# Kernel tuning notes

Measured on AMD Instinct MI355X. Metric: run time of the kernel, lower is better.

The kernel has to match this reference:

```python
import jax, jax.numpy as jnp
import numpy as np

B = 16
Dv, Hv, Wv = 128, 128, 128   # patchsize voxel grid (C=1)
NPTS = 1920                  # 16*120 points
EPS_IN = 1e-5                # InstanceNorm eps


def _inorm(x):
    # InstanceNorm1d, affine=False: normalize over last (length) dim per (b, c)
    m = jnp.mean(x, axis=-1, keepdims=True)
    v = jnp.var(x, axis=-1, keepdims=True)
    return (x - m) * jax.lax.rsqrt(v + EPS_IN)


def _mlp(q, w1, b1, w2, b2, w3, b3, w4, b4, w5, b5):
    b = q.shape[0]
    x = q.reshape(b, 256, 8)                                    # (b, 2048//8, 8)
    x = jnp.einsum('bil,oi->bol', x, w1) + b1[None, :, None]    # Conv1d(256,240,1) -> (b,240,8)
    x = jax.nn.relu(_inorm(x.reshape(b, 64, 30)))               # view (b,64,30), IN(64)
    # Conv1d(64,128,1,groups=64): each in-ch -> 2 out-chs; then view (b,32,120)
    x = (x[:, :, None, :] * w2[None, :, :, None] + b2.reshape(1, 64, 2, 1)).reshape(b, 32, 120)
    x = jax.nn.relu(_inorm(x))
    # Conv1d(32,64,1,groups=32); view (b,16,480)
    x = (x[:, :, None, :] * w3[None, :, :, None] + b3.reshape(1, 32, 2, 1)).reshape(b, 16, 480)
    x = jax.nn.relu(_inorm(x))
    # Conv1d(16,64,1,groups=16); view (b,16,1920)
    x = (x[:, :, None, :] * w4[None, :, :, None] + b4.reshape(1, 16, 4, 1)).reshape(b, 16, 1920)
    x = jax.nn.relu(_inorm(x))
    return jnp.einsum('bil,oi->bol', x, w5) + b5[None, :, None]  # Conv1d(16,3,1) -> (b,3,1920)


def _splat(vals, grid):
    # True adjoint of 3D grid_sample (align_corners=False, zeros padding):
    # trilinear scatter-add of point values into the voxel grid.
    # vals: (b, N); grid: (b, N, 3) with (x, y, z) ~ (W, H, D) normalized coords.
    b, n = vals.shape
    px = ((grid[..., 0] + 1.0) * Wv - 1.0) * 0.5
    py = ((grid[..., 1] + 1.0) * Hv - 1.0) * 0.5
    pz = ((grid[..., 2] + 1.0) * Dv - 1.0) * 0.5
    x0f = jnp.floor(px); y0f = jnp.floor(py); z0f = jnp.floor(pz)
    fx = px - x0f; fy = py - y0f; fz = pz - z0f
    x0 = x0f.astype(jnp.int32); y0 = y0f.astype(jnp.int32); z0 = z0f.astype(jnp.int32)
    bidx = jnp.arange(b, dtype=jnp.int32)[:, None]
    out = jnp.zeros(b * Dv * Hv * Wv, dtype=vals.dtype)
    for dz in (0, 1):
        wz = fz if dz else (1.0 - fz)
        for dy in (0, 1):
            wy = fy if dy else (1.0 - fy)
            for dx in (0, 1):
                wx = fx if dx else (1.0 - fx)
                xi = x0 + dx; yi = y0 + dy; zi = z0 + dz
                w = wx * wy * wz * vals
                valid = (xi >= 0) & (xi < Wv) & (yi >= 0) & (yi < Hv) & (zi >= 0) & (zi < Dv)
                w = jnp.where(valid, w, 0.0)
                xi = jnp.clip(xi, 0, Wv - 1)
                yi = jnp.clip(yi, 0, Hv - 1)
                zi = jnp.clip(zi, 0, Dv - 1)
                flat = ((bidx * Dv + zi) * Hv + yi) * Wv + xi
                out = out.at[flat.ravel()].add(w.ravel())
    return out.reshape(b, 1, Dv, Hv, Wv)


def _avgpool3(x):
    # AvgPool3d(3, stride=1, padding=1, count_include_pad=True) as separable 1D averages
    for ax in (2, 3, 4):
        pad = [(1, 1) if i == ax else (0, 0) for i in range(5)]
        xp = jnp.pad(x, pad)
        n = x.shape[ax]
        x = (jax.lax.slice_in_dim(xp, 0, n, axis=ax)
             + jax.lax.slice_in_dim(xp, 1, n + 1, axis=ax)
             + jax.lax.slice_in_dim(xp, 2, n + 2, axis=ax)) / 3.0
    return x


def _smooth(x):
    return _avgpool3(_avgpool3(_avgpool3(x)))


def _forward(q, q_val, w1, b1, w2, b2, w3, b3, w4, b4, w5, b5):
    b = q.shape[0]
    q3 = _mlp(q, w1, b1, w2, b2, w3, b3, w4, b4, w5, b5)   # (b, 3, 1920)
    coords = jnp.tanh(q3)                                    # q0_coord
    grid = jnp.transpose(coords, (0, 2, 1))                  # (b, 1920, 3)
    vals = jnp.broadcast_to(jax.nn.sigmoid(q_val).reshape(1, NPTS), (b, NPTS))
    out = _splat(vals, grid)
    out0 = _splat(jnp.ones((b, NPTS), q.dtype), grid)
    return _smooth(out) / (_smooth(out0) + 0.001)


def setup_inputs() -> dict:
    key = jax.random.key(0)
    ks = jax.random.split(key, 12)
    sc = 0.1
    return {
        'q': jax.random.normal(ks[0], (B, 2048), jnp.float32),
        'q_val': jax.random.normal(ks[1], (1, 1, 16, 120), jnp.float32),
        'w1': jax.random.normal(ks[2], (240, 256), jnp.float32) * sc,
        'b1': jax.random.normal(ks[3], (240,), jnp.float32) * sc,
        'w2': jax.random.normal(ks[4], (64, 2), jnp.float32) * sc,
        'b2': jax.random.normal(ks[5], (128,), jnp.float32) * sc,
        'w3': jax.random.normal(ks[6], (32, 2), jnp.float32) * sc,
        'b3': jax.random.normal(ks[7], (64,), jnp.float32) * sc,
        'w4': jax.random.normal(ks[8], (16, 4), jnp.float32) * sc,
        'b4': jax.random.normal(ks[9], (64,), jnp.float32) * sc,
        'w5': jax.random.normal(ks[10], (3, 16), jnp.float32) * sc,
        'b5': jax.random.normal(ks[11], (3,), jnp.float32) * sc,
    }


def reference(q, q_val, w1, b1, w2, b2, w3, b3, w4, b4, w5, b5):
    return _forward(q, q_val, w1, b1, w2, b2, w3, b3, w4, b4, w5, b5)
```

## Files before the change

### kernel.cpp

```cpp
#include <hip/hip_runtime.h>
#include <cstddef>

#define NB 16
#define NVOX 128
#define NPT 1920

static __device__ __forceinline__ float2 f2(float a, float b) {
    float2 r; r.x = a; r.y = b; return r;
}

__device__ __forceinline__ void coef(int g, float& cm1, float& c0, float& cp1)
{
    cm1 = (g == 1 || g == 127) ? 5.f : 6.f;
    c0  = (g == 0 || g == 127) ? 4.f : 7.f;
    cp1 = (g == 0 || g == 126) ? 5.f : 6.f;
}

__global__ __launch_bounds__(256)
void zero_out(float4* __restrict__ out)
{
    int idx = blockIdx.x * 2048 + threadIdx.x;
    #pragma unroll
    for (int i = 0; i < 8; ++i)
        out[idx + i * 256] = make_float4(0.f, 0.f, 0.f, 0.f);
}

__global__ __launch_bounds__(1024)
void tail_k(const float* __restrict__ q, const float* __restrict__ w1,
            const float* __restrict__ b1, const float* __restrict__ qval,
            const float* __restrict__ w2, const float* __restrict__ b2,
            const float* __restrict__ w3, const float* __restrict__ b3,
            const float* __restrict__ w4, const float* __restrict__ b4,
            const float* __restrict__ w5, const float* __restrict__ b5,
            float4* __restrict__ pts, int* __restrict__ bcount,
            int* __restrict__ list)
{
    __shared__ float x1s[1920];
    __shared__ float h3[7680];
    __shared__ float m4s[16], r4s[16];
    __shared__ unsigned char lflags[2048];
    __shared__ int lcount;

    const int b = blockIdx.x;
    const int t = threadIdx.x;
    float* qs = h3;

    for (int u = t; u < 2048; u += 1024) {
        qs[u] = q[b * 2048 + u];
        lflags[u] = 0;
    }
    if (t == 0) lcount = 0;
    __syncthreads();

    for (int u = t; u < 1920; u += 1024) {
        int o = u >> 3, l = u & 7;
        const float4* wr = (const float4*)(w1 + o * 256);
        float acc = 0.f;
        #pragma unroll 8
        for (int i4 = 0; i4 < 64; ++i4) {
            float4 w = wr[i4];
            int base = i4 * 32 + l;
            acc = fmaf(w.x, qs[base],      acc);
            acc = fmaf(w.y, qs[base + 8],  acc);
            acc = fmaf(w.z, qs[base + 16], acc);
            acc = fmaf(w.w, qs[base + 24], acc);
        }
        x1s[u] = b1[o] + acc;
    }
    __syncthreads();

    const int l = t & 63;
    const int c1l = l >> 4;
    const int p16 = l & 15;
    const bool hasb = (p16 < 14);
    {
        const int c3 = t >> 6;
        const int c1 = 4 * c3 + c1l;
        const float* xrow = x1s + c1 * 30;
        float a0 = xrow[p16];
        float a1 = hasb ? xrow[p16 + 16] : 0.f;

        float s = a0 + a1, s2 = a0 * a0 + a1 * a1;
        #pragma unroll
        for (int m = 1; m <= 8; m <<= 1) {
            s  += __shfl_xor(s,  m);
            s2 += __shfl_xor(s2, m);
        }
        float mean = s * (1.f / 30.f);
        float var  = s2 * (1.f / 30.f) - mean * mean;
        float rstd = rsqrtf(var + 1e-5f);
        a0 = fmaxf((a0 - mean) * rstd, 0.f);
        a1 = fmaxf((a1 - mean) * rstd, 0.f);

        const float w20 = w2[c1 * 2 + 0], w21 = w2[c1 * 2 + 1];
        const float b20 = b2[c1 * 2 + 0], b21 = b2[c1 * 2 + 1];
        float y00 = fmaf(a0, w20, b20), y01 = fmaf(a0, w21, b21);
        float y10 = fmaf(a1, w20, b20), y11 = fmaf(a1, w21, b21);

        float u1 = y00 + y01 + (hasb ? (y10 + y11) : 0.f);
        float u2 = y00 * y00 + y01 * y01
                 + (hasb ? (y10 * y10 + y11 * y11) : 0.f);
        #pragma unroll
        for (int m = 1; m <= 16; m <<= 1) {
            u1 += __shfl_xor(u1, m);
            u2 += __shfl_xor(u2, m);
        }
        mean = u1 * (1.f / 120.f);
        var  = u2 * (1.f / 120.f) - mean * mean;
        rstd = rsqrtf(var + 1e-5f);
        y00 = fmaxf((y00 - mean) * rstd, 0.f);
        y01 = fmaxf((y01 - mean) * rstd, 0.f);
        y10 = fmaxf((y10 - mean) * rstd, 0.f);
        y11 = fmaxf((y11 - mean) * rstd, 0.f);

        const int c2 = c1 >> 1;
        const float w30 = w3[c2 * 2 + 0], w31 = w3[c2 * 2 + 1];
        const float b30 = b3[c2 * 2 + 0], b31 = b3[c2 * 2 + 1];
        float z000 = fmaf(y00, w30, b30), z001 = fmaf(y00, w31, b31);
        float z010 = fmaf(y01, w30, b30), z011 = fmaf(y01, w31, b31);
        float z100 = fmaf(y10, w30, b30), z101 = fmaf(y10, w31, b31);
        float z110 = fmaf(y11, w30, b30), z111 = fmaf(y11, w31, b31);

        float v1 = z000 + z001 + z010 + z011
                 + (hasb ? (z100 + z101 + z110 + z111) : 0.f);
        float v2 = z000 * z000 + z001 * z001 + z010 * z010 + z011 * z011
                 + (hasb ? (z100 * z100 + z101 * z101
                          + z110 * z110 + z111 * z111) : 0.f);
        #pragma unroll
        for (int m = 1; m <= 32; m <<= 1) {
            v1 += __shfl_xor(v1, m);
            v2 += __shfl_xor(v2, m);
        }
        mean = v1 * (1.f / 480.f);
        var  = v2 * (1.f / 480.f) - mean * mean;
        rstd = rsqrtf(var + 1e-5f);

        const int qb0 = (c1l >> 1) * 240;
        const int pb0 = (c1l & 1) * 60;
        float* hw = h3 + c3 * 480;
        float s4 = 0.f, q4 = 0.f;
        {
            float v;
            v = fmaxf((z000 - mean) * rstd, 0.f); hw[qb0 +       pb0 +      p16] = v; s4 += v; q4 += v * v;
            v = fmaxf((z001 - mean) * rstd, 0.f); hw[qb0 + 120 + pb0 +      p16] = v; s4 += v; q4 += v * v;
            v = fmaxf((z010 - mean) * rstd, 0.f); hw[qb0 +       pb0 + 30 + p16] = v; s4 += v; q4 += v * v;
            v = fmaxf((z011 - mean) * rstd, 0.f); hw[qb0 + 120 + pb0 + 30 + p16] = v; s4 += v; q4 += v * v;
            if (hasb) {
                v = fmaxf((z100 - mean) * rstd, 0.f); hw[qb0 +       pb0 +      p16 + 16] = v; s4 += v; q4 += v * v;
                v = fmaxf((z101 - mean) * rstd, 0.f); hw[qb0 + 120 + pb0 +      p16 + 16] = v; s4 += v; q4 += v * v;
                v = fmaxf((z110 - mean) * rstd, 0.f); hw[qb0 +       pb0 + 30 + p16 + 16] = v; s4 += v; q4 += v * v;
                v = fmaxf((z111 - mean) * rstd, 0.f); hw[qb0 + 120 + pb0 + 30 + p16 + 16] = v; s4 += v; q4 += v * v;
            }
        }
        #pragma unroll
        for (int m = 1; m <= 32; m <<= 1) {
            s4 += __shfl_xor(s4, m);
            q4 += __shfl_xor(q4, m);
        }
        if (l == 0) {
            float sum4 = 0.f, sq4 = 0.f;
            #pragma unroll
            for (int j = 0; j < 4; ++j) {
                float ww = w4[c3 * 4 + j], bb = b4[c3 * 4 + j];
                sum4 += ww * s4 + 480.f * bb;
                sq4  += ww * ww * q4 + 2.f * ww * bb * s4 + 480.f * bb * bb;
            }
            float m4 = sum4 * (1.f / 1920.f);
            float var4 = sq4 * (1.f / 1920.f) - m4 * m4;
            m4s[c3] = m4; r4s[c3] = rsqrtf(var4 + 1e-5f);
        }
    }
    __syncthreads();

    for (int p = t; p < NPT; p += 1024) {
        int j = p / 480;
        int pp = p - j * 480;
        float a0e = b5[0], a1e = b5[1], a2e = b5[2];
        #pragma unroll
        for (int c = 0; c < 16; ++c) {
            float xv = h3[c * 480 + pp];
            float x4 = fmaf(xv, w4[c * 4 + j], b4[c * 4 + j]);
            float h  = fmaxf((x4 - m4s[c]) * r4s[c], 0.f);
            a0e = fmaf(w5[c],      h, a0e);
            a1e = fmaf(w5[16 + c], h, a1e);
            a2e = fmaf(w5[32 + c], h, a2e);
        }
        float px = tanhf(a0e) * 64.f + 63.5f;
        float py = tanhf(a1e) * 64.f + 63.5f;
        float pz = tanhf(a2e) * 64.f + 63.5f;
        float val = 1.f / (1.f + expf(-qval[p]));

        float4 pv; pv.x = px; pv.y = py; pv.z = pz; pv.w = val;
        pts[b * NPT + p] = pv;

        int x0 = (int)floorf(px), y0 = (int)floorf(py), z0 = (int)floorf(pz);
        int xlo = max(0, x0 - 3), xhi = min(127, x0 + 4);
        int ylo = max(0, y0 - 3), yhi = min(127, y0 + 4);
        int zlo = max(0, z0 - 3), zhi = min(127, z0 + 4);
        if (xlo > xhi || ylo > yhi || zlo > zhi) continue;
        int pxl = xlo >> 4, pxh = xhi >> 4;
        int tyl = ylo >> 3, tyh = yhi >> 3;
        int tzl = zlo >> 3, tzh = zhi >> 3;
        for (int tz = tzl; tz <= tzh; ++tz)
            for (int ty = tyl; ty <= tyh; ++ty)
                for (int px2 = pxl; px2 <= pxh; ++px2)
                    lflags[(tz * 16 + ty) * 8 + px2] = 1;
    }
    __syncthreads();

    for (int u = t; u < 2048; u += 1024) {
        if (lflags[u]) {
            int pos = atomicAdd(&lcount, 1);
            list[b * 2048 + pos] = (b << 11) | u;
        }
    }
    __syncthreads();
    if (t == 0) bcount[b] = lcount;
}

__device__ __forceinline__ void decode_tile(const int* pf, const int* __restrict__ list,
                                            int idx, int& Tx, int& Ty, int& Tz, int& pb_)
{
    int bb = 0;
    #pragma unroll 1
    for (; bb < 15; ++bb) if (idx < pf[bb + 1]) break;
    int code = list[bb * 2048 + (idx - pf[bb])];
    pb_ = code >> 11;
    Tx = (code & 7) * 16;
    Ty = ((code >> 3) & 15) * 8;
    Tz = ((code >> 7) & 15) * 8;
}

__device__ __forceinline__ void zero_buf(float2* raw, int th, int stride)
{
    float4* rz = (float4*)raw;
    for (int u = th; u < 2156; u += stride)
        rz[u] = make_float4(0.f, 0.f, 0.f, 0.f);
}

__device__ __forceinline__ void scatter(float2* raw, const float4* __restrict__ pbp,
                                        int lo, int hi, int th, int stride,
                                        int Tx, int Ty, int Tz)
{
    for (int p = lo + th; p < hi; p += stride) {
        float4 pt = pbp[p];
        float x0f = floorf(pt.x), y0f = floorf(pt.y), z0f = floorf(pt.z);
        int x0 = (int)x0f, y0 = (int)y0f, z0 = (int)z0f;
        int lx0 = x0 - Tx + 3, ly0 = y0 - Ty + 3, lz0 = z0 - Tz + 3;
        if (lx0 + 1 < 0 || lx0 > 21 || ly0 + 1 < 0 || ly0 > 13 ||
            lz0 + 1 < 0 || lz0 > 13) continue;
        float fx = pt.x - x0f, fy = pt.y - y0f, fz = pt.z - z0f;
        float val = pt.w;
        #pragma unroll
        for (int dz = 0; dz < 2; ++dz) {
            int zi = z0 + dz, lz = lz0 + dz;
            if ((unsigned)zi >= 128u || (unsigned)lz >= 14u) continue;
            float wz = dz ? fz : 1.f - fz;
            #pragma unroll
            for (int dy = 0; dy < 2; ++dy) {
                int yi = y0 + dy, ly = ly0 + dy;
                if ((unsigned)yi >= 128u || (unsigned)ly >= 14u) continue;
                float wy = dy ? fy : 1.f - fy;
                #pragma unroll
                for (int dx = 0; dx < 2; ++dx) {
                    int xi = x0 + dx, lx = lx0 + dx;
                    if ((unsigned)xi >= 128u || (unsigned)lx >= 22u) continue;
                    float w = (dx ? fx : 1.f - fx) * wy * wz;
                    float2* cell = &raw[(lz * 14 + ly) * 22 + lx];
                    atomicAdd(&cell->x, w * val);
                    atomicAdd(&cell->y, w);
                }
            }
        }
    }
}

__device__ __forceinline__ void zpass(float2* raw, int Tz, int th)
{
    for (int c = th; c < 308; c += 256) {
        float2 w0 = raw[c],            w1_ = raw[c + 308],
               w2_ = raw[c + 2 * 308], w3_ = raw[c + 3 * 308],
               w4_ = raw[c + 4 * 308], w5_ = raw[c + 5 * 308],
               w6_ = raw[c + 6 * 308];
        #pragma unroll
        for (int z = 0; z < 8; ++z) {
            float cm1, c0, cp1; coef(Tz + z, cm1, c0, cp1);
            float sx = (w0.x + w6_.x) + 3.f * (w1_.x + w5_.x)
                     + cm1 * w2_.x + c0 * w3_.x + cp1 * w4_.x;
            float sy = (w0.y + w6_.y) + 3.f * (w1_.y + w5_.y)
                     + cm1 * w2_.y + c0 * w3_.y + cp1 * w4_.y;
            float2 nxt = raw[c + ((z < 7) ? z + 7 : 7) * 308];
            raw[c + z * 308] = f2(sx * (1.f / 27.f), sy * (1.f / 27.f));
            w0 = w1_; w1_ = w2_; w2_ = w3_; w3_ = w4_; w4_ = w5_; w5_ = w6_; w6_ = nxt;
        }
    }
}

__device__ __forceinline__ void ypass(float2* raw, int Ty, int th)
{
    if (th < 176) {
        int z = th / 22, lx = th - z * 22;
        float2* base = &raw[z * 308 + lx];
        float2 w0 = base[0],       w1_ = base[22],
               w2_ = base[2 * 22], w3_ = base[3 * 22],
               w4_ = base[4 * 22], w5_ = base[5 * 22],
               w6_ = base[6 * 22];
        #pragma unroll
        for (int y = 0; y < 8; ++y) {
            float cm1, c0, cp1; coef(Ty + y, cm1, c0, cp1);
            float sx = (w0.x + w6_.x) + 3.f * (w1_.x + w5_.x)
                     + cm1 * w2_.x + c0 * w3_.x + cp1 * w4_.x;
            float sy = (w0.y + w6_.y) + 3.f * (w1_.y + w5_.y)
                     + cm1 * w2_.y + c0 * w3_.y + cp1 * w4_.y;
            float2 nxt = base[((y < 7) ? y + 7 : 7) * 22];
            base[y * 22] = f2(sx * (1.f / 27.f), sy * (1.f / 27.f));
            w0 = w1_; w1_ = w2_; w2_ = w3_; w3_ = w4_; w4_ = w5_; w5_ = w6_; w6_ = nxt;
        }
    }
}

__device__ __forceinline__ void xpass(float2* raw, int Tx, float* __restrict__ ob, int th)
{
    if (th < 128) {
        int row = th >> 1, hx = th & 1;
        int z = row >> 3, y = row & 7;
        const float2* a = &raw[z * 308 + y * 22 + hx * 8];
        float2 w0 = a[0], w1_ = a[1], w2_ = a[2], w3_ = a[3],
               w4_ = a[4], w5_ = a[5], w6_ = a[6];
        float res[8];
        #pragma unroll
        for (int i = 0; i < 8; ++i) {
            int x = hx * 8 + i;
            float cm1, c0, cp1; coef(Tx + x, cm1, c0, cp1);
            float sx = (w0.x + w6_.x) + 3.f * (w1_.x + w5_.x)
                     + cm1 * w2_.x + c0 * w3_.x + cp1 * w4_.x;
            float sy = (w0.y + w6_.y) + 3.f * (w1_.y + w5_.y)
                     + cm1 * w2_.y + c0 * w3_.y + cp1 * w4_.y;
            res[i] = (sx * (1.f / 27.f)) / (sy * (1.f / 27.f) + 0.001f);
            float2 nxt = a[(i < 7) ? i + 7 : 13];
            w0 = w1_; w1_ = w2_; w2_ = w3_; w3_ = w4_; w4_ = w5_; w5_ = w6_; w6_ = nxt;
        }
        float* orow = &ob[((size_t)z * NVOX + y) * NVOX + hx * 8];
        *(float4*)&orow[0] = make_float4(res[0], res[1], res[2], res[3]);
        *(float4*)&orow[4] = make_float4(res[4], res[5], res[6], res[7]);
    }
}

__global__ __launch_bounds__(512, 4)
void tile_k(const float4* __restrict__ pts, const int* __restrict__ bcount,
            const int* __restrict__ list, float* __restrict__ out)
{
    __shared__ float2 bufA[4312];
    __shared__ float2 bufB[4312];
    __shared__ int pf[17];

    const int t = threadIdx.x;
    if (t < 16) pf[t + 1] = bcount[t];
    if (t == 0) pf[0] = 0;
    __syncthreads();
    if (t == 0) {
        int s = 0;
        #pragma unroll
        for (int i = 1; i <= 16; ++i) { s += pf[i]; pf[i] = s; }
    }
    __syncthreads();

    const int total = pf[16];
    const int grid = gridDim.x;
    const int chunk = (total + grid - 1) / grid;
    int idx = blockIdx.x * chunk;
    const int end = min(idx + chunk, total);
    if (idx >= end) return;

    int cTx, cTy, cTz, cPb;
    decode_tile(pf, list, idx, cTx, cTy, cTz, cPb);
    float2* cur = bufA;
    float2* nxt = bufB;

    zero_buf(cur, t, 512);
    __syncthreads();
    scatter(cur, pts + cPb * NPT, 0, NPT, t, 512, cTx, cTy, cTz);
    __syncthreads();

    const int w8 = t >> 6;
    const bool low = (w8 < 4);
    const int th = t & 255;

    while (true) {
        const bool have_next = (idx + 1) < end;
        int nTx = 0, nTy = 0, nTz = 0, nPb = 0;
        if (have_next)
            decode_tile(pf, list, idx + 1, nTx, nTy, nTz, nPb);

        if (low) zpass(cur, cTz, th);
        else if (have_next) zero_buf(nxt, th, 256);
        __syncthreads();

        if (low) ypass(cur, cTy, th);
        else if (have_next)
            scatter(nxt, pts + nPb * NPT, 0, 960, th, 256, nTx, nTy, nTz);
        __syncthreads();

        if (low) {
            float* ob = out + (((size_t)(cPb * NVOX + cTz) * NVOX + cTy) * NVOX + cTx);
            xpass(cur, cTx, ob, th);
        } else if (have_next)
            scatter(nxt, pts + nPb * NPT, 960, NPT, th, 256, nTx, nTy, nTz);
        __syncthreads();

        if (!have_next) break;
        ++idx;
        float2* tmp = cur; cur = nxt; nxt = tmp;
        cTx = nTx; cTy = nTy; cTz = nTz; cPb = nPb;
    }
}

extern "C" void kernel_launch(void* const* d_in, const int* in_sizes, int n_in,
                              void* d_out, int out_size, void* d_ws, size_t ws_size,
                              hipStream_t stream)
{
    const float* q    = (const float*)d_in[0];
    const float* qval = (const float*)d_in[1];
    const float* w1   = (const float*)d_in[2];
    const float* b1   = (const float*)d_in[3];
    const float* w2   = (const float*)d_in[4];
    const float* b2   = (const float*)d_in[5];
    const float* w3   = (const float*)d_in[6];
    const float* b3   = (const float*)d_in[7];
    const float* w4   = (const float*)d_in[8];
    const float* b4   = (const float*)d_in[9];
    const float* w5   = (const float*)d_in[10];
    const float* b5   = (const float*)d_in[11];
    float* out = (float*)d_out;

    int*    bcount = (int*)d_ws;
    int*    list   = (int*)((char*)d_ws + 64);
    float4* pts    = (float4*)((char*)d_ws + 131136);

    zero_out<<<4096, 256, 0, stream>>>((float4*)out);

    tail_k<<<NB, 1024, 0, stream>>>(q, w1, b1, qval, w2, b2, w3, b3,
                                    w4, b4, w5, b5, pts, bcount, list);

    tile_k<<<512, 512, 0, stream>>>(pts, bcount, list, out);
}
```

Baseline: 242.7 us.

## Bin points per tile with CSR lists and fuse output zeroing into tail kernel

The tail kernel now counts points per output tile, builds prefix offsets and per-tile point index lists (CSR), so the tile kernel scatters only the relevant points instead of scanning all 1920 points per tile. The separate zeroing kernel is folded into extra blocks of the tail kernel, and the double-buffered producer/consumer tile pipeline is replaced by a simpler single-buffer loop with a larger grid. This cuts redundant point loads and bounds checks and one launch, at the cost of shared atomics for binning, extra workspace and the loss of scatter/filter overlap.

```diff
diff --git a/kernel.cpp b/kernel.cpp
--- a/kernel.cpp
+++ b/kernel.cpp
@@ -16,38 +16,42 @@
     cp1 = (g == 0 || g == 126) ? 5.f : 6.f;
 }
 
-__global__ __launch_bounds__(256)
-void zero_out(float4* __restrict__ out)
+__global__ __launch_bounds__(1024)
+void tail_zero_k(const float* __restrict__ q, const float* __restrict__ w1,
+                 const float* __restrict__ b1, const float* __restrict__ qval,
+                 const float* __restrict__ w2, const float* __restrict__ b2,
+                 const float* __restrict__ w3, const float* __restrict__ b3,
+                 const float* __restrict__ w4, const float* __restrict__ b4,
+                 const float* __restrict__ w5, const float* __restrict__ b5,
+                 float4* __restrict__ pts, int* __restrict__ bcount,
+                 int* __restrict__ list, int* __restrict__ rp,
+                 int* __restrict__ ent, float4* __restrict__ out4)
 {
-    int idx = blockIdx.x * 2048 + threadIdx.x;
-    #pragma unroll
-    for (int i = 0; i < 8; ++i)
-        out[idx + i * 256] = make_float4(0.f, 0.f, 0.f, 0.f);
-}
-
-__global__ __launch_bounds__(1024)
-void tail_k(const float* __restrict__ q, const float* __restrict__ w1,
-            const float* __restrict__ b1, const float* __restrict__ qval,
-            const float* __restrict__ w2, const float* __restrict__ b2,
-            const float* __restrict__ w3, const float* __restrict__ b3,
-            const float* __restrict__ w4, const float* __restrict__ b4,
-            const float* __restrict__ w5, const float* __restrict__ b5,
-            float4* __restrict__ pts, int* __restrict__ bcount,
-            int* __restrict__ list)
-{
+    const int bid = blockIdx.x;
+    const int t = threadIdx.x;
+
+    if (bid >= NB) {
+        const int stride = 496 * 1024;
+        for (int i = (bid - NB) * 1024 + t; i < (NB * NVOX * NVOX * NVOX) / 4;
+             i += stride)
+            out4[i] = make_float4(0.f, 0.f, 0.f, 0.f);
+        return;
+    }
+
     __shared__ float x1s[1920];
     __shared__ float h3[7680];
     __shared__ float m4s[16], r4s[16];
-    __shared__ unsigned char lflags[2048];
+    __shared__ int cnt[2048];
+    __shared__ int off[2048];
+    __shared__ int gsum[64];
     __shared__ int lcount;
 
-    const int b = blockIdx.x;
-    const int t = threadIdx.x;
+    const int b = bid;
     float* qs = h3;
 
     for (int u = t; u < 2048; u += 1024) {
         qs[u] = q[b * 2048 + u];
-        lflags[u] = 0;
+        cnt[u] = 0;
     }
     if (t == 0) lcount = 0;
     __syncthreads();
@@ -172,7 +176,11 @@
     }
     __syncthreads();
 
-    for (int p = t; p < NPT; p += 1024) {
+    int x0s[2], y0s[2], z0s[2];
+    #pragma unroll
+    for (int k = 0; k < 2; ++k) {
+        int p = t + k * 1024;
+        if (p >= NPT) break;
         int j = p / 480;
         int pp = p - j * 480;
         float a0e = b5[0], a1e = b5[1], a2e = b5[2];
@@ -194,22 +202,63 @@
         pts[b * NPT + p] = pv;
 
         int x0 = (int)floorf(px), y0 = (int)floorf(py), z0 = (int)floorf(pz);
+        x0s[k] = x0; y0s[k] = y0; z0s[k] = z0;
         int xlo = max(0, x0 - 3), xhi = min(127, x0 + 4);
         int ylo = max(0, y0 - 3), yhi = min(127, y0 + 4);
         int zlo = max(0, z0 - 3), zhi = min(127, z0 + 4);
-        if (xlo > xhi || ylo > yhi || zlo > zhi) continue;
         int pxl = xlo >> 4, pxh = xhi >> 4;
         int tyl = ylo >> 3, tyh = yhi >> 3;
         int tzl = zlo >> 3, tzh = zhi >> 3;
         for (int tz = tzl; tz <= tzh; ++tz)
             for (int ty = tyl; ty <= tyh; ++ty)
                 for (int px2 = pxl; px2 <= pxh; ++px2)
-                    lflags[(tz * 16 + ty) * 8 + px2] = 1;
-    }
-    __syncthreads();
-
+                    atomicAdd(&cnt[(tz * 16 + ty) * 8 + px2], 1);
+    }
+    __syncthreads();
+
+    if (t < 64) {
+        int s = 0;
+        for (int i = 0; i < 32; ++i) s += cnt[t * 32 + i];
+        gsum[t] = s;
+    }
+    __syncthreads();
+    if (t == 0) {
+        int s = 0;
+        for (int i = 0; i < 64; ++i) { int v = gsum[i]; gsum[i] = s; s += v; }
+    }
+    __syncthreads();
+    if (t < 64) {
+        int s = gsum[t];
+        for (int i = 0; i < 32; ++i) {
+            int u = t * 32 + i;
+            rp[b * 2049 + u] = s;
+            off[u] = s;
+            s += cnt[u];
+        }
+        if (t == 63) rp[b * 2049 + 2048] = s;
+    }
+    __syncthreads();
+
+    #pragma unroll
+    for (int k = 0; k < 2; ++k) {
+        int p = t + k * 1024;
+        if (p >= NPT) break;
+        int x0 = x0s[k], y0 = y0s[k], z0 = z0s[k];
+        int xlo = max(0, x0 - 3), xhi = min(127, x0 + 4);
+        int ylo = max(0, y0 - 3), yhi = min(127, y0 + 4);
+        int zlo = max(0, z0 - 3), zhi = min(127, z0 + 4);
+        int pxl = xlo >> 4, pxh = xhi >> 4;
+        int tyl = ylo >> 3, tyh = yhi >> 3;
+        int tzl = zlo >> 3, tzh = zhi >> 3;
+        for (int tz = tzl; tz <= tzh; ++tz)
+            for (int ty = tyl; ty <= tyh; ++ty)
+                for (int px2 = pxl; px2 <= pxh; ++px2) {
+                    int pos = atomicAdd(&off[(tz * 16 + ty) * 8 + px2], 1);
+                    ent[b * 16384 + pos] = p;
+                }
+    }
     for (int u = t; u < 2048; u += 1024) {
-        if (lflags[u]) {
+        if (cnt[u] > 0) {
             int pos = atomicAdd(&lcount, 1);
             list[b * 2048 + pos] = (b << 11) | u;
         }
@@ -218,140 +267,12 @@
     if (t == 0) bcount[b] = lcount;
 }
 
-__device__ __forceinline__ void decode_tile(const int* pf, const int* __restrict__ list,
-                                            int idx, int& Tx, int& Ty, int& Tz, int& pb_)
+__global__ __launch_bounds__(512, 8)
+void tile_k(const float4* __restrict__ pts, const int* __restrict__ bcount,
+            const int* __restrict__ list, const int* __restrict__ rp,
+            const int* __restrict__ ent, float* __restrict__ out)
 {
-    int bb = 0;
-    #pragma unroll 1
-    for (; bb < 15; ++bb) if (idx < pf[bb + 1]) break;
-    int code = list[bb * 2048 + (idx - pf[bb])];
-    pb_ = code >> 11;
-    Tx = (code & 7) * 16;
-    Ty = ((code >> 3) & 15) * 8;
-    Tz = ((code >> 7) & 15) * 8;
-}
-
-__device__ __forceinline__ void zero_buf(float2* raw, int th, int stride)
-{
-    float4* rz = (float4*)raw;
-    for (int u = th; u < 2156; u += stride)
-        rz[u] = make_float4(0.f, 0.f, 0.f, 0.f);
-}
-
-__device__ __forceinline__ void scatter(float2* raw, const float4* __restrict__ pbp,
-                                        int lo, int hi, int th, int stride,
-                                        int Tx, int Ty, int Tz)
-{
-    for (int p = lo + th; p < hi; p += stride) {
-        float4 pt = pbp[p];
-        float x0f = floorf(pt.x), y0f = floorf(pt.y), z0f = floorf(pt.z);
-        int x0 = (int)x0f, y0 = (int)y0f, z0 = (int)z0f;
-        int lx0 = x0 - Tx + 3, ly0 = y0 - Ty + 3, lz0 = z0 - Tz + 3;
-        if (lx0 + 1 < 0 || lx0 > 21 || ly0 + 1 < 0 || ly0 > 13 ||
-            lz0 + 1 < 0 || lz0 > 13) continue;
-        float fx = pt.x - x0f, fy = pt.y - y0f, fz = pt.z - z0f;
-        float val = pt.w;
-        #pragma unroll
-        for (int dz = 0; dz < 2; ++dz) {
-            int zi = z0 + dz, lz = lz0 + dz;
-            if ((unsigned)zi >= 128u || (unsigned)lz >= 14u) continue;
-            float wz = dz ? fz : 1.f - fz;
-            #pragma unroll
-            for (int dy = 0; dy < 2; ++dy) {
-                int yi = y0 + dy, ly = ly0 + dy;
-                if ((unsigned)yi >= 128u || (unsigned)ly >= 14u) continue;
-                float wy = dy ? fy : 1.f - fy;
-                #pragma unroll
-                for (int dx = 0; dx < 2; ++dx) {
-                    int xi = x0 + dx, lx = lx0 + dx;
-                    if ((unsigned)xi >= 128u || (unsigned)lx >= 22u) continue;
-                    float w = (dx ? fx : 1.f - fx) * wy * wz;
-                    float2* cell = &raw[(lz * 14 + ly) * 22 + lx];
-                    atomicAdd(&cell->x, w * val);
-                    atomicAdd(&cell->y, w);
-                }
-            }
-        }
-    }
-}
-
-__device__ __forceinline__ void zpass(float2* raw, int Tz, int th)
-{
-    for (int c = th; c < 308; c += 256) {
-        float2 w0 = raw[c],            w1_ = raw[c + 308],
-               w2_ = raw[c + 2 * 308], w3_ = raw[c + 3 * 308],
-               w4_ = raw[c + 4 * 308], w5_ = raw[c + 5 * 308],
-               w6_ = raw[c + 6 * 308];
-        #pragma unroll
-        for (int z = 0; z < 8; ++z) {
-            float cm1, c0, cp1; coef(Tz + z, cm1, c0, cp1);
-            float sx = (w0.x + w6_.x) + 3.f * (w1_.x + w5_.x)
-                     + cm1 * w2_.x + c0 * w3_.x + cp1 * w4_.x;
-            float sy = (w0.y + w6_.y) + 3.f * (w1_.y + w5_.y)
-                     + cm1 * w2_.y + c0 * w3_.y + cp1 * w4_.y;
-            float2 nxt = raw[c + ((z < 7) ? z + 7 : 7) * 308];
-            raw[c + z * 308] = f2(sx * (1.f / 27.f), sy * (1.f / 27.f));
-            w0 = w1_; w1_ = w2_; w2_ = w3_; w3_ = w4_; w4_ = w5_; w5_ = w6_; w6_ = nxt;
-        }
-    }
-}
-
-__device__ __forceinline__ void ypass(float2* raw, int Ty, int th)
-{
-    if (th < 176) {
-        int z = th / 22, lx = th - z * 22;
-        float2* base = &raw[z * 308 + lx];
-        float2 w0 = base[0],       w1_ = base[22],
-               w2_ = base[2 * 22], w3_ = base[3 * 22],
-               w4_ = base[4 * 22], w5_ = base[5 * 22],
-               w6_ = base[6 * 22];
-        #pragma unroll
-        for (int y = 0; y < 8; ++y) {
-            float cm1, c0, cp1; coef(Ty + y, cm1, c0, cp1);
-            float sx = (w0.x + w6_.x) + 3.f * (w1_.x + w5_.x)
-                     + cm1 * w2_.x + c0 * w3_.x + cp1 * w4_.x;
-            float sy = (w0.y + w6_.y) + 3.f * (w1_.y + w5_.y)
-                     + cm1 * w2_.y + c0 * w3_.y + cp1 * w4_.y;
-            float2 nxt = base[((y < 7) ? y + 7 : 7) * 22];
-            base[y * 22] = f2(sx * (1.f / 27.f), sy * (1.f / 27.f));
-            w0 = w1_; w1_ = w2_; w2_ = w3_; w3_ = w4_; w4_ = w5_; w5_ = w6_; w6_ = nxt;
-        }
-    }
-}
-
-__device__ __forceinline__ void xpass(float2* raw, int Tx, float* __restrict__ ob, int th)
-{
-    if (th < 128) {
-        int row = th >> 1, hx = th & 1;
-        int z = row >> 3, y = row & 7;
-        const float2* a = &raw[z * 308 + y * 22 + hx * 8];
-        float2 w0 = a[0], w1_ = a[1], w2_ = a[2], w3_ = a[3],
-               w4_ = a[4], w5_ = a[5], w6_ = a[6];
-        float res[8];
-        #pragma unroll
-        for (int i = 0; i < 8; ++i) {
-            int x = hx * 8 + i;
-            float cm1, c0, cp1; coef(Tx + x, cm1, c0, cp1);
-            float sx = (w0.x + w6_.x) + 3.f * (w1_.x + w5_.x)
-                     + cm1 * w2_.x + c0 * w3_.x + cp1 * w4_.x;
-            float sy = (w0.y + w6_.y) + 3.f * (w1_.y + w5_.y)
-                     + cm1 * w2_.y + c0 * w3_.y + cp1 * w4_.y;
-            res[i] = (sx * (1.f / 27.f)) / (sy * (1.f / 27.f) + 0.001f);
-            float2 nxt = a[(i < 7) ? i + 7 : 13];
-            w0 = w1_; w1_ = w2_; w2_ = w3_; w3_ = w4_; w4_ = w5_; w5_ = w6_; w6_ = nxt;
-        }
-        float* orow = &ob[((size_t)z * NVOX + y) * NVOX + hx * 8];
-        *(float4*)&orow[0] = make_float4(res[0], res[1], res[2], res[3]);
-        *(float4*)&orow[4] = make_float4(res[4], res[5], res[6], res[7]);
-    }
-}
-
-__global__ __launch_bounds__(512, 4)
-void tile_k(const float4* __restrict__ pts, const int* __restrict__ bcount,
-            const int* __restrict__ list, float* __restrict__ out)
-{
-    __shared__ float2 bufA[4312];
-    __shared__ float2 bufB[4312];
+    __shared__ float2 raw[4312];
     __shared__ int pf[17];
 
     const int t = threadIdx.x;
@@ -364,54 +285,124 @@
         for (int i = 1; i <= 16; ++i) { s += pf[i]; pf[i] = s; }
     }
     __syncthreads();
-
     const int total = pf[16];
-    const int grid = gridDim.x;
-    const int chunk = (total + grid - 1) / grid;
-    int idx = blockIdx.x * chunk;
-    const int end = min(idx + chunk, total);
-    if (idx >= end) return;
-
-    int cTx, cTy, cTz, cPb;
-    decode_tile(pf, list, idx, cTx, cTy, cTz, cPb);
-    float2* cur = bufA;
-    float2* nxt = bufB;
-
-    zero_buf(cur, t, 512);
-    __syncthreads();
-    scatter(cur, pts + cPb * NPT, 0, NPT, t, 512, cTx, cTy, cTz);
-    __syncthreads();
-
-    const int w8 = t >> 6;
-    const bool low = (w8 < 4);
-    const int th = t & 255;
-
-    while (true) {
-        const bool have_next = (idx + 1) < end;
-        int nTx = 0, nTy = 0, nTz = 0, nPb = 0;
-        if (have_next)
-            decode_tile(pf, list, idx + 1, nTx, nTy, nTz, nPb);
-
-        if (low) zpass(cur, cTz, th);
-        else if (have_next) zero_buf(nxt, th, 256);
+
+    for (int idx = blockIdx.x; idx < total; idx += gridDim.x) {
+        int bb = 0;
+        #pragma unroll 1
+        for (; bb < 15; ++bb) if (idx < pf[bb + 1]) break;
+        const int code = list[bb * 2048 + (idx - pf[bb])];
+        const int u    = code & 2047;
+        const int pb_  = code >> 11;
+        const int Tx = (code & 7) * 16;
+        const int Ty = ((code >> 3) & 15) * 8;
+        const int Tz = ((code >> 7) & 15) * 8;
+        const int base = rp[pb_ * 2049 + u];
+        const int endp = rp[pb_ * 2049 + u + 1];
+        float* ob = out + (((size_t)(pb_ * NVOX + Tz) * NVOX + Ty) * NVOX + Tx);
+
+        {
+            float4* rz = (float4*)raw;
+            for (int v = t; v < 2156; v += 512) rz[v] = make_float4(0.f, 0.f, 0.f, 0.f);
+        }
         __syncthreads();
 
-        if (low) ypass(cur, cTy, th);
-        else if (have_next)
-            scatter(nxt, pts + nPb * NPT, 0, 960, th, 256, nTx, nTy, nTz);
+        for (int e = base + t; e < endp; e += 512) {
+            int p = ent[pb_ * 16384 + e];
+            float4 pt = pts[pb_ * NPT + p];
+            float x0f = floorf(pt.x), y0f = floorf(pt.y), z0f = floorf(pt.z);
+            int x0 = (int)x0f, y0 = (int)y0f, z0 = (int)z0f;
+            int lx0 = x0 - Tx + 3, ly0 = y0 - Ty + 3, lz0 = z0 - Tz + 3;
+            float fx = pt.x - x0f, fy = pt.y - y0f, fz = pt.z - z0f;
+            float val = pt.w;
+            #pragma unroll
+            for (int dz = 0; dz < 2; ++dz) {
+                int zi = z0 + dz, lz = lz0 + dz;
+                if ((unsigned)zi >= 128u || (unsigned)lz >= 14u) continue;
+                float wz = dz ? fz : 1.f - fz;
+                #pragma unroll
+                for (int dy = 0; dy < 2; ++dy) {
+                    int yi = y0 + dy, ly = ly0 + dy;
+                    if ((unsigned)yi >= 128u || (unsigned)ly >= 14u) continue;
+                    float wy = dy ? fy : 1.f - fy;
+                    #pragma unroll
+                    for (int dx = 0; dx < 2; ++dx) {
+                        int xi = x0 + dx, lx = lx0 + dx;
+                        if ((unsigned)xi >= 128u || (unsigned)lx >= 22u) continue;
+                        float w = (dx ? fx : 1.f - fx) * wy * wz;
+                        float2* cell = &raw[(lz * 14 + ly) * 22 + lx];
+                        atomicAdd(&cell->x, w * val);
+                        atomicAdd(&cell->y, w);
+                    }
+                }
+            }
+        }
         __syncthreads();
 
-        if (low) {
-            float* ob = out + (((size_t)(cPb * NVOX + cTz) * NVOX + cTy) * NVOX + cTx);
-            xpass(cur, cTx, ob, th);
-        } else if (have_next)
-            scatter(nxt, pts + nPb * NPT, 960, NPT, th, 256, nTx, nTy, nTz);
+        if (t < 308) {
+            float2 w0 = raw[t],            w1_ = raw[t + 308],
+                   w2_ = raw[t + 2 * 308], w3_ = raw[t + 3 * 308],
+                   w4_ = raw[t + 4 * 308], w5_ = raw[t + 5 * 308],
+                   w6_ = raw[t + 6 * 308];
+            #pragma unroll
+            for (int z = 0; z < 8; ++z) {
+                float cm1, c0, cp1; coef(Tz + z, cm1, c0, cp1);
+                float sx = (w0.x + w6_.x) + 3.f * (w1_.x + w5_.x)
+                         + cm1 * w2_.x + c0 * w3_.x + cp1 * w4_.x;
+                float sy = (w0.y + w6_.y) + 3.f * (w1_.y + w5_.y)
+                         + cm1 * w2_.y + c0 * w3_.y + cp1 * w4_.y;
+                float2 nxt = raw[t + ((z < 7) ? z + 7 : 7) * 308];
+                raw[t + z * 308] = f2(sx * (1.f / 27.f), sy * (1.f / 27.f));
+                w0 = w1_; w1_ = w2_; w2_ = w3_; w3_ = w4_; w4_ = w5_; w5_ = w6_; w6_ = nxt;
+            }
+        }
         __syncthreads();
 
-        if (!have_next) break;
-        ++idx;
-        float2* tmp = cur; cur = nxt; nxt = tmp;
-        cTx = nTx; cTy = nTy; cTz = nTz; cPb = nPb;
+        if (t < 176) {
+            int z = t / 22, lx = t - z * 22;
+            float2* base2 = &raw[z * 308 + lx];
+            float2 w0 = base2[0],       w1_ = base2[22],
+                   w2_ = base2[2 * 22], w3_ = base2[3 * 22],
+                   w4_ = base2[4 * 22], w5_ = base2[5 * 22],
+                   w6_ = base2[6 * 22];
+            #pragma unroll
+            for (int y = 0; y < 8; ++y) {
+                float cm1, c0, cp1; coef(Ty + y, cm1, c0, cp1);
+                float sx = (w0.x + w6_.x) + 3.f * (w1_.x + w5_.x)
+                         + cm1 * w2_.x + c0 * w3_.x + cp1 * w4_.x;
+                float sy = (w0.y + w6_.y) + 3.f * (w1_.y + w5_.y)
+                         + cm1 * w2_.y + c0 * w3_.y + cp1 * w4_.y;
+                float2 nxt = base2[((y < 7) ? y + 7 : 7) * 22];
+                base2[y * 22] = f2(sx * (1.f / 27.f), sy * (1.f / 27.f));
+                w0 = w1_; w1_ = w2_; w2_ = w3_; w3_ = w4_; w4_ = w5_; w5_ = w6_; w6_ = nxt;
+            }
+        }
+        __syncthreads();
+
+        if (t < 128) {
+            int row = t >> 1, hx = t & 1;
+            int z = row >> 3, y = row & 7;
+            const float2* a = &raw[z * 308 + y * 22 + hx * 8];
+            float2 w0 = a[0], w1_ = a[1], w2_ = a[2], w3_ = a[3],
+                   w4_ = a[4], w5_ = a[5], w6_ = a[6];
+            float res[8];
+            #pragma unroll
+            for (int i = 0; i < 8; ++i) {
+                int x = hx * 8 + i;
+                float cm1, c0, cp1; coef(Tx + x, cm1, c0, cp1);
+                float sx = (w0.x + w6_.x) + 3.f * (w1_.x + w5_.x)
+                         + cm1 * w2_.x + c0 * w3_.x + cp1 * w4_.x;
+                float sy = (w0.y + w6_.y) + 3.f * (w1_.y + w5_.y)
+                         + cm1 * w2_.y + c0 * w3_.y + cp1 * w4_.y;
+                res[i] = (sx * (1.f / 27.f)) / (sy * (1.f / 27.f) + 0.001f);
+                float2 nxt = a[(i < 7) ? i + 7 : 13];
+                w0 = w1_; w1_ = w2_; w2_ = w3_; w3_ = w4_; w4_ = w5_; w5_ = w6_; w6_ = nxt;
+            }
+            float* orow = &ob[((size_t)z * NVOX + y) * NVOX + hx * 8];
+            *(float4*)&orow[0] = make_float4(res[0], res[1], res[2], res[3]);
+            *(float4*)&orow[4] = make_float4(res[4], res[5], res[6], res[7]);
+        }
+        __syncthreads();
     }
 }
 
@@ -435,12 +426,13 @@
 
     int*    bcount = (int*)d_ws;
     int*    list   = (int*)((char*)d_ws + 64);
-    float4* pts    = (float4*)((char*)d_ws + 131136);
-
-    zero_out<<<4096, 256, 0, stream>>>((float4*)out);
-
-    tail_k<<<NB, 1024, 0, stream>>>(q, w1, b1, qval, w2, b2, w3, b3,
-                                    w4, b4, w5, b5, pts, bcount, list);
-
-    tile_k<<<512, 512, 0, stream>>>(pts, bcount, list, out);
+    int*    rp     = (int*)((char*)d_ws + 131136);
+    int*    ent    = (int*)((char*)d_ws + 262272);
+    float4* pts    = (float4*)((char*)d_ws + 1310848);
+
+    tail_zero_k<<<512, 1024, 0, stream>>>(q, w1, b1, qval, w2, b2, w3, b3,
+                                          w4, b4, w5, b5, pts, bcount, list,
+                                          rp, ent, (float4*)out);
+
+    tile_k<<<1024, 512, 0, stream>>>(pts, bcount, list, rp, ent, out);
 }
```

Measured after the change: 235.9 us. 2.8% less time.
